# Kernel optimization log

Measured on AMD Instinct MI355X. Metric: run time of the kernel, lower is better.

## Reference

```python
import jax, jax.numpy as jnp
import numpy as np


def setup_inputs() -> dict:
    key = jax.random.key(0)
    kx, kg = jax.random.split(key)
    x = jax.random.normal(kx, (16, 512, 64, 64), dtype=jnp.float32)
    gamma = jax.random.normal(kg, (1,), dtype=jnp.float32)
    return {"x": x, "gamma": gamma}


def reference(x, gamma):
    B, C, H, W = x.shape
    q = x.reshape(B, C, H * W)                      # [B, C, N]
    # energy[b, c, d] = <channel c, channel d> over spatial positions
    energy = jnp.einsum('bcn,bdn->bcd', q, q)       # [B, C, C]
    # max-centering softmax: softmax(rowmax(energy) - energy)
    energy_new = jnp.max(energy, axis=-1, keepdims=True) - energy
    attention = jax.nn.softmax(energy_new, axis=-1)  # [B, C, C]
    out = jnp.einsum('bcd,bdn->bcn', attention, q).reshape(B, C, H, W)
    return gamma * out + x
```

## Files before the change

kernel.cpp:

```cpp
#include <hip/hip_runtime.h>


#define BATCH 16
#define CCH   512
#define NSP   4096

typedef __attribute__((ext_vector_type(8))) short bfx8;
typedef __attribute__((ext_vector_type(4))) short bfx4;
typedef __attribute__((ext_vector_type(4))) float fx4;
typedef __attribute__((ext_vector_type(2))) float fx2;

__device__ __forceinline__ short f2bf(float v) {
    union { float f; unsigned u; } a; a.f = v;
    unsigned r = a.u + 0x7fffu + ((a.u >> 16) & 1u);
    return (short)(r >> 16);
}
__device__ __forceinline__ float bf2f(short s) {
    union { unsigned u; float f; } a; a.u = ((unsigned)(unsigned short)s) << 16;
    return a.f;
}

__device__ __forceinline__ void gload16(const short* g, short* l) {
    __builtin_amdgcn_global_load_lds((const __attribute__((address_space(1))) void*)g,
                                     (__attribute__((address_space(3))) void*)l, 16, 0, 0);
}

__global__ __launch_bounds__(256) void split_kernel(const float* __restrict__ x,
                                                    short* __restrict__ xh,
                                                    short* __restrict__ xl) {
    size_t stride = (size_t)gridDim.x * 256;
    size_t total8 = (size_t)BATCH * CCH * NSP / 8;
    for (size_t u = (size_t)blockIdx.x * 256 + threadIdx.x; u < total8; u += stride) {
        size_t i = u * 8;
        fx4 a = *(const fx4*)(x + i);
        fx4 b = *(const fx4*)(x + i + 4);
        bfx8 h, l;
#pragma unroll
        for (int e = 0; e < 4; ++e) {
            short ha = f2bf(a[e]); h[e]     = ha; l[e]     = f2bf(a[e] - bf2f(ha));
            short hb = f2bf(b[e]); h[e + 4] = hb; l[e + 4] = f2bf(b[e] - bf2f(hb));
        }
        *(bfx8*)(xh + i) = h;
        *(bfx8*)(xl + i) = l;
    }
}

__global__ __launch_bounds__(256) void energy_kernel(const short* __restrict__ xh,
                                                     const short* __restrict__ xl,
                                                     float* __restrict__ energy) {
    int orig = blockIdx.x;
    int wgid = (orig & 7) * 72 + (orig >> 3);
    int b = wgid / 36;
    int t = wgid % 36;
    int ti = 0, rem = t;
    while (rem >= 8 - ti) { rem -= 8 - ti; ++ti; }
    int tj = ti + rem;
    int c0 = ti * 64, d0 = tj * 64;
    bool diag = (ti == tj);
    const short* qh = xh + (size_t)b * CCH * NSP;
    const short* ql = xl + (size_t)b * CCH * NSP;

    __shared__ short S[2][4][64][32];

    int tid  = threadIdx.x;
    int lane = tid & 63;
    int w    = tid >> 6;
    int wr   = (w >> 1) * 32;
    int wc   = (w & 1) * 32;

    int rb   = w * 16;
    int srow = lane >> 2;
    int gch  = (lane & 3) ^ ((lane >> 3) & 3);

    auto STAGE = [&](int buf, int kt) {
        size_t koff = (size_t)kt * 32 + gch * 8;
        gload16(qh + (size_t)(c0 + rb + srow) * NSP + koff, &S[buf][0][rb][0]);
        gload16(ql + (size_t)(c0 + rb + srow) * NSP + koff, &S[buf][1][rb][0]);
        if (!diag) {
            gload16(qh + (size_t)(d0 + rb + srow) * NSP + koff, &S[buf][2][rb][0]);
            gload16(ql + (size_t)(d0 + rb + srow) * NSP + koff, &S[buf][3][rb][0]);
        }
    };

    fx4 acc[2][2];
#pragma unroll
    for (int i = 0; i < 2; i++)
#pragma unroll
        for (int j = 0; j < 2; j++) acc[i][j] = (fx4)(0.0f);

    STAGE(0, 0);
    __syncthreads();

    const char* Sb = (const char*)&S[0][0][0][0];
    const int bmH = diag ? 0 : 2, bmL = diag ? 1 : 3;
    int h = lane >> 4;
    int cur = 0;
    const int NT = NSP / 32;
    for (int kt = 0; kt < NT; ++kt) {
        bfx8 ah_[2], al_[2], bh_[2], bl_[2];
        const char* Sc = Sb + cur * (4 * 64 * 64);
#pragma unroll
        for (int mi = 0; mi < 2; ++mi) {
            int r  = wr + mi * 16 + (lane & 15);
            int bo = r * 64 + ((h ^ ((r >> 1) & 3)) << 4);
            ah_[mi] = *(const bfx8*)(Sc + 0 * 4096 + bo);
            al_[mi] = *(const bfx8*)(Sc + 1 * 4096 + bo);
        }
#pragma unroll
        for (int ni = 0; ni < 2; ++ni) {
            int r  = wc + ni * 16 + (lane & 15);
            int bo = r * 64 + ((h ^ ((r >> 1) & 3)) << 4);
            bh_[ni] = *(const bfx8*)(Sc + bmH * 4096 + bo);
            bl_[ni] = *(const bfx8*)(Sc + bmL * 4096 + bo);
        }
        if (kt + 1 < NT) STAGE(cur ^ 1, kt + 1);
#pragma unroll
        for (int mi = 0; mi < 2; ++mi)
#pragma unroll
            for (int ni = 0; ni < 2; ++ni) {
                acc[mi][ni] = __builtin_amdgcn_mfma_f32_16x16x32_bf16(ah_[mi], bh_[ni], acc[mi][ni], 0, 0, 0);
                acc[mi][ni] = __builtin_amdgcn_mfma_f32_16x16x32_bf16(ah_[mi], bl_[ni], acc[mi][ni], 0, 0, 0);
                acc[mi][ni] = __builtin_amdgcn_mfma_f32_16x16x32_bf16(al_[mi], bh_[ni], acc[mi][ni], 0, 0, 0);
            }
        __syncthreads();
        cur ^= 1;
    }

    int colw = lane & 15;
    int rowg = (lane >> 4) * 4;
#pragma unroll
    for (int mi = 0; mi < 2; ++mi)
#pragma unroll
        for (int ni = 0; ni < 2; ++ni) {
            int cb = c0 + wr + mi * 16 + rowg;
            int d  = d0 + wc + ni * 16 + colw;
#pragma unroll
            for (int r = 0; r < 4; ++r) {
                int c = cb + r;
                float v = acc[mi][ni][r];
                energy[((size_t)b * CCH + c) * CCH + d] = v;
                if (!diag)
                    energy[((size_t)b * CCH + d) * CCH + c] = v;
            }
        }
}

__global__ __launch_bounds__(256) void softmax_kernel(float* __restrict__ energy) {
    size_t row = blockIdx.x;
    float* e = energy + row * CCH;
    int tid = threadIdx.x;
    fx2 v = *(const fx2*)(e + 2 * tid);

    float m = fminf(v[0], v[1]);
#pragma unroll
    for (int off = 32; off; off >>= 1) m = fminf(m, __shfl_xor(m, off));
    __shared__ float redm[4];
    __shared__ float reds[4];
    if ((tid & 63) == 0) redm[tid >> 6] = m;
    __syncthreads();
    m = fminf(fminf(redm[0], redm[1]), fminf(redm[2], redm[3]));

    float w0 = __expf(m - v[0]);
    float w1 = __expf(m - v[1]);
    float s = w0 + w1;
#pragma unroll
    for (int off = 32; off; off >>= 1) s += __shfl_xor(s, off);
    if ((tid & 63) == 0) reds[tid >> 6] = s;
    __syncthreads();
    s = (reds[0] + reds[1]) + (reds[2] + reds[3]);
    float inv = 1.0f / s;
    unsigned uw = ((unsigned)(unsigned short)f2bf(w0 * inv)) |
                  (((unsigned)(unsigned short)f2bf(w1 * inv)) << 16);
    ((unsigned*)e)[tid] = uw;
}

__global__ __launch_bounds__(256, 2) void out_kernel(const float* __restrict__ x,
                                                     const short* __restrict__ xh,
                                                     const short* __restrict__ attnb,
                                                     const float* __restrict__ gamma,
                                                     float* __restrict__ out) {
    int orig = blockIdx.x;
    int blk  = (orig & 7) * 256 + (orig >> 3);
    int b   = blk >> 7;
    int t   = blk & 127;
    int c0  = (t >> 5) * 128;
    int n0  = (t & 31) * 128;
    const float* xb = x + (size_t)b * CCH * NSP;
    const short* qh = xh + (size_t)b * CCH * NSP;
    const short* ab = attnb + (size_t)b * CCH * 1024;

    __shared__ short As[128][40];
    __shared__ short Bs[128][32];
    char* bbase = (char*)&Bs[0][0];

    int tid  = threadIdx.x;
    int lane = tid & 63;
    int w    = tid >> 6;
    int wr   = (w >> 1) * 64;
    int wc   = (w & 1) * 64;

    int ar = tid >> 1, ac = (tid & 1) * 16;
    int p   = tid & 63;
    int db  = tid >> 6;
    int ne  = 2 * p;
    int sw0 = (ne ^ (ne >> 2)) & 3;
    int sw1 = ((ne + 1) ^ ((ne + 1) >> 2)) & 3;
    int addrE = ne * 64 + ((db ^ sw0) << 4);
    int addrO = (ne + 1) * 64 + ((db ^ sw1) << 4);
    bool podd = (p & 1);

    fx4 acc[4][4];
#pragma unroll
    for (int i = 0; i < 4; i++)
#pragma unroll
        for (int j = 0; j < 4; j++) acc[i][j] = (fx4)(0.0f);

    bfx8 areg0 = *(const bfx8*)(ab + (size_t)(c0 + ar) * 1024 + ac);
    bfx8 areg1 = *(const bfx8*)(ab + (size_t)(c0 + ar) * 1024 + ac + 8);
    unsigned wv[8];
    {
        const short* src = qh + (size_t)(db * 8) * NSP + n0 + ne;
#pragma unroll
        for (int i = 0; i < 8; ++i) wv[i] = *(const unsigned*)(src + (size_t)i * NSP);
    }

    for (int kt = 0; kt < CCH / 32; ++kt) {
        __syncthreads();
        *(bfx8*)&As[ar][ac]     = areg0;
        *(bfx8*)&As[ar][ac + 8] = areg1;
        {
            bfx8 p0, p1;
#pragma unroll
            for (int i = 0; i < 8; ++i) { p0[i] = (short)(wv[i] & 0xffff); p1[i] = (short)(wv[i] >> 16); }
            int a1 = podd ? addrO : addrE;
            int a2 = podd ? addrE : addrO;
            bfx8 v1 = podd ? p1 : p0;
            bfx8 v2 = podd ? p0 : p1;
            *(bfx8*)(bbase + a1) = v1;
            *(bfx8*)(bbase + a2) = v2;
        }
        __syncthreads();
        if (kt + 1 < CCH / 32) {
            areg0 = *(const bfx8*)(ab + (size_t)(c0 + ar) * 1024 + (kt + 1) * 32 + ac);
            areg1 = *(const bfx8*)(ab + (size_t)(c0 + ar) * 1024 + (kt + 1) * 32 + ac + 8);
            const short* src = qh + (size_t)((kt + 1) * 32 + db * 8) * NSP + n0 + ne;
#pragma unroll
            for (int i = 0; i < 8; ++i) wv[i] = *(const unsigned*)(src + (size_t)i * NSP);
        }

        bfx8 af[4];
#pragma unroll
        for (int mi = 0; mi < 4; ++mi)
            af[mi] = *(const bfx8*)&As[wr + mi * 16 + (lane & 15)][(lane >> 4) * 8];
        bfx8 bf[4];
#pragma unroll
        for (int ni = 0; ni < 4; ++ni) {
            int n   = wc + ni * 16 + (lane & 15);
            int swn = (n ^ (n >> 2)) & 3;
            bf[ni] = *(const bfx8*)(bbase + n * 64 + (((lane >> 4) ^ swn) << 4));
        }
#pragma unroll
        for (int mi = 0; mi < 4; ++mi)
#pragma unroll
            for (int ni = 0; ni < 4; ++ni)
                acc[mi][ni] = __builtin_amdgcn_mfma_f32_16x16x32_bf16(af[mi], bf[ni], acc[mi][ni], 0, 0, 0);
    }

    float g = gamma[0];
    int colw = lane & 15;
    int rowg = (lane >> 4) * 4;
#pragma unroll
    for (int mi = 0; mi < 4; ++mi)
#pragma unroll
        for (int ni = 0; ni < 4; ++ni) {
            int n = n0 + wc + ni * 16 + colw;
#pragma unroll
            for (int r = 0; r < 4; ++r) {
                int c = c0 + wr + mi * 16 + rowg + r;
                size_t off = ((size_t)b * CCH + c) * NSP + n;
                out[off] = g * acc[mi][ni][r] + xb[(size_t)c * NSP + n];
            }
        }
}

extern "C" void kernel_launch(void* const* d_in, const int* in_sizes, int n_in,
                              void* d_out, int out_size, void* d_ws, size_t ws_size,
                              hipStream_t stream) {
    (void)in_sizes; (void)n_in; (void)out_size; (void)ws_size;
    const float* x     = (const float*)d_in[0];
    const float* gamma = (const float*)d_in[1];
    float*       out   = (float*)d_out;

    size_t nel  = (size_t)BATCH * CCH * NSP;
    size_t bfsz = nel * sizeof(short);
    short* xhp    = (short*)d_ws;
    short* xlp    = (short*)((char*)d_ws + bfsz);
    float* energy = (float*)((char*)d_ws + 2 * bfsz);

    split_kernel  <<<2048, 256, 0, stream>>>(x, xhp, xlp);
    energy_kernel <<<BATCH * 36, 256, 0, stream>>>(xhp, xlp, energy);
    softmax_kernel<<<BATCH * CCH, 256, 0, stream>>>(energy);
    out_kernel    <<<BATCH * 128, 256, 0, stream>>>(x, xhp, (const short*)energy, gamma, out);
}
```

Measured before the change: 234.9 us.

## Pre-transpose bf16 x and double-buffer out_kernel with direct global-to-LDS loads

After: 255.3 us. 8.7% more time.

```diff
diff --git a/kernel.cpp b/kernel.cpp
--- a/kernel.cpp
+++ b/kernel.cpp
@@ -145,6 +145,44 @@
         }
 }
 
+__global__ __launch_bounds__(256) void transpose_kernel(const short* __restrict__ xh,
+                                                        short* __restrict__ xt) {
+    int blk = blockIdx.x;
+    int b  = blk >> 9;
+    int t  = blk & 511;
+    int ct = t >> 6;
+    int nt = t & 63;
+    int c0 = ct * 64, n0 = nt * 64;
+    const short* src = xh + (size_t)b * CCH * NSP;
+    short*       dst = xt + (size_t)b * NSP * CCH;
+
+    __shared__ short Lt[64][64];
+
+    int tid = threadIdx.x;
+    int p  = tid & 31;
+    int dr = tid >> 5;
+
+    unsigned wv[8];
+    const short* sp = src + (size_t)(c0 + dr * 8) * NSP + n0 + 2 * p;
+#pragma unroll
+    for (int i = 0; i < 8; ++i) wv[i] = *(const unsigned*)(sp + (size_t)i * NSP);
+    bfx8 q0, q1;
+#pragma unroll
+    for (int i = 0; i < 8; ++i) { q0[i] = (short)(wv[i] & 0xffff); q1[i] = (short)(wv[i] >> 16); }
+    int slot = dr ^ (p & 7);
+    *(bfx8*)(&Lt[0][0] + (2 * p) * 64 + slot * 8)     = q0;
+    *(bfx8*)(&Lt[0][0] + (2 * p + 1) * 64 + slot * 8) = q1;
+    __syncthreads();
+
+#pragma unroll
+    for (int it = 0; it < 2; ++it) {
+        int n  = it * 32 + (tid >> 3);
+        int ch = tid & 7;
+        bfx8 v = *(const bfx8*)(&Lt[0][0] + n * 64 + (ch ^ ((n >> 1) & 7)) * 8);
+        *(bfx8*)(dst + (size_t)(n0 + n) * CCH + c0 + ch * 8) = v;
+    }
+}
+
 __global__ __launch_bounds__(256) void softmax_kernel(float* __restrict__ energy) {
     size_t row = blockIdx.x;
     float* e = energy + row * CCH;
@@ -174,9 +212,9 @@
     ((unsigned*)e)[tid] = uw;
 }
 
-__global__ __launch_bounds__(256, 2) void out_kernel(const float* __restrict__ x,
-                                                     const short* __restrict__ xh,
+__global__ __launch_bounds__(256, 3) void out_kernel(const float* __restrict__ x,
                                                      const short* __restrict__ attnb,
+                                                     const short* __restrict__ xt,
                                                      const float* __restrict__ gamma,
                                                      float* __restrict__ out) {
     int orig = blockIdx.x;
@@ -186,12 +224,11 @@
     int c0  = (t >> 5) * 128;
     int n0  = (t & 31) * 128;
     const float* xb = x + (size_t)b * CCH * NSP;
-    const short* qh = xh + (size_t)b * CCH * NSP;
     const short* ab = attnb + (size_t)b * CCH * 1024;
-
-    __shared__ short As[128][40];
-    __shared__ short Bs[128][32];
-    char* bbase = (char*)&Bs[0][0];
+    const short* qt = xt + (size_t)b * NSP * CCH;
+
+    __shared__ short SA[2][128][32];
+    __shared__ short SB[2][128][32];
 
     int tid  = threadIdx.x;
     int lane = tid & 63;
@@ -199,15 +236,17 @@
     int wr   = (w >> 1) * 64;
     int wc   = (w & 1) * 64;
 
-    int ar = tid >> 1, ac = (tid & 1) * 16;
-    int p   = tid & 63;
-    int db  = tid >> 6;
-    int ne  = 2 * p;
-    int sw0 = (ne ^ (ne >> 2)) & 3;
-    int sw1 = ((ne + 1) ^ ((ne + 1) >> 2)) & 3;
-    int addrE = ne * 64 + ((db ^ sw0) << 4);
-    int addrO = (ne + 1) * 64 + ((db ^ sw1) << 4);
-    bool podd = (p & 1);
+    int srow = lane >> 2;
+    int gch  = (lane & 3) ^ ((lane >> 3) & 3);
+
+    auto STAGE = [&](int buf, int kt) {
+#pragma unroll
+        for (int hf = 0; hf < 2; ++hf) {
+            int rg = hf * 64 + w * 16;
+            gload16(ab + (size_t)(c0 + rg + srow) * 1024 + kt * 32 + gch * 8, &SA[buf][rg][0]);
+            gload16(qt + (size_t)(n0 + rg + srow) * 512  + kt * 32 + gch * 8, &SB[buf][rg][0]);
+        }
+    };
 
     fx4 acc[4][4];
 #pragma unroll
@@ -215,55 +254,32 @@
 #pragma unroll
         for (int j = 0; j < 4; j++) acc[i][j] = (fx4)(0.0f);
 
-    bfx8 areg0 = *(const bfx8*)(ab + (size_t)(c0 + ar) * 1024 + ac);
-    bfx8 areg1 = *(const bfx8*)(ab + (size_t)(c0 + ar) * 1024 + ac + 8);
-    unsigned wv[8];
-    {
-        const short* src = qh + (size_t)(db * 8) * NSP + n0 + ne;
-#pragma unroll
-        for (int i = 0; i < 8; ++i) wv[i] = *(const unsigned*)(src + (size_t)i * NSP);
-    }
-
-    for (int kt = 0; kt < CCH / 32; ++kt) {
-        __syncthreads();
-        *(bfx8*)&As[ar][ac]     = areg0;
-        *(bfx8*)&As[ar][ac + 8] = areg1;
-        {
-            bfx8 p0, p1;
-#pragma unroll
-            for (int i = 0; i < 8; ++i) { p0[i] = (short)(wv[i] & 0xffff); p1[i] = (short)(wv[i] >> 16); }
-            int a1 = podd ? addrO : addrE;
-            int a2 = podd ? addrE : addrO;
-            bfx8 v1 = podd ? p1 : p0;
-            bfx8 v2 = podd ? p0 : p1;
-            *(bfx8*)(bbase + a1) = v1;
-            *(bfx8*)(bbase + a2) = v2;
-        }
-        __syncthreads();
-        if (kt + 1 < CCH / 32) {
-            areg0 = *(const bfx8*)(ab + (size_t)(c0 + ar) * 1024 + (kt + 1) * 32 + ac);
-            areg1 = *(const bfx8*)(ab + (size_t)(c0 + ar) * 1024 + (kt + 1) * 32 + ac + 8);
-            const short* src = qh + (size_t)((kt + 1) * 32 + db * 8) * NSP + n0 + ne;
-#pragma unroll
-            for (int i = 0; i < 8; ++i) wv[i] = *(const unsigned*)(src + (size_t)i * NSP);
-        }
-
-        bfx8 af[4];
-#pragma unroll
-        for (int mi = 0; mi < 4; ++mi)
-            af[mi] = *(const bfx8*)&As[wr + mi * 16 + (lane & 15)][(lane >> 4) * 8];
-        bfx8 bf[4];
+    STAGE(0, 0);
+    __syncthreads();
+
+    int h = lane >> 4;
+    int cur = 0;
+    const int NT = CCH / 32;
+    for (int kt = 0; kt < NT; ++kt) {
+        bfx8 af[4], bf[4];
+#pragma unroll
+        for (int mi = 0; mi < 4; ++mi) {
+            int r  = wr + mi * 16 + (lane & 15);
+            af[mi] = *(const bfx8*)((const char*)&SA[cur][0][0] + r * 64 + ((h ^ ((r >> 1) & 3)) << 4));
+        }
 #pragma unroll
         for (int ni = 0; ni < 4; ++ni) {
-            int n   = wc + ni * 16 + (lane & 15);
-            int swn = (n ^ (n >> 2)) & 3;
-            bf[ni] = *(const bfx8*)(bbase + n * 64 + (((lane >> 4) ^ swn) << 4));
-        }
+            int r  = wc + ni * 16 + (lane & 15);
+            bf[ni] = *(const bfx8*)((const char*)&SB[cur][0][0] + r * 64 + ((h ^ ((r >> 1) & 3)) << 4));
+        }
+        if (kt + 1 < NT) STAGE(cur ^ 1, kt + 1);
 #pragma unroll
         for (int mi = 0; mi < 4; ++mi)
 #pragma unroll
             for (int ni = 0; ni < 4; ++ni)
                 acc[mi][ni] = __builtin_amdgcn_mfma_f32_16x16x32_bf16(af[mi], bf[ni], acc[mi][ni], 0, 0, 0);
+        __syncthreads();
+        cur ^= 1;
     }
 
     float g = gamma[0];
@@ -297,8 +313,9 @@
     short* xlp    = (short*)((char*)d_ws + bfsz);
     float* energy = (float*)((char*)d_ws + 2 * bfsz);
 
-    split_kernel  <<<2048, 256, 0, stream>>>(x, xhp, xlp);
-    energy_kernel <<<BATCH * 36, 256, 0, stream>>>(xhp, xlp, energy);
-    softmax_kernel<<<BATCH * CCH, 256, 0, stream>>>(energy);
-    out_kernel    <<<BATCH * 128, 256, 0, stream>>>(x, xhp, (const short*)energy, gamma, out);
-}
+    split_kernel     <<<2048, 256, 0, stream>>>(x, xhp, xlp);
+    energy_kernel    <<<BATCH * 36, 256, 0, stream>>>(xhp, xlp, energy);
+    transpose_kernel <<<BATCH * 512, 256, 0, stream>>>(xhp, xlp);
+    softmax_kernel   <<<BATCH * CCH, 256, 0, stream>>>(energy);
+    out_kernel       <<<BATCH * 128, 256, 0, stream>>>(x, (const short*)energy, xlp, gamma, out);
+}
```
